# Kernel optimization log

Measured on AMD Instinct MI355X. Metric: run time of the kernel, lower is better.

Reference implementation:

```python
import jax, jax.numpy as jnp
import numpy as np

D_MODEL = 1024
N_HEADS = 16
HEAD_DIM = D_MODEL // N_HEADS


def setup_inputs() -> dict:
    key = jax.random.key(0)
    ks = jax.random.split(key, 9)
    B, S, D = 2, 2048, D_MODEL
    scale = 1.0 / np.sqrt(D)
    return {
        "q": jax.random.normal(ks[0], (B, S, D), jnp.float32),
        "k": jax.random.normal(ks[1], (B, S, D), jnp.float32),
        "v": jax.random.normal(ks[2], (B, S, D), jnp.float32),
        "Wq": jax.random.normal(ks[3], (D, D), jnp.float32) * scale,
        "bq": jax.random.normal(ks[4], (D,), jnp.float32) * 0.01,
        "Wk": jax.random.normal(ks[5], (D, D), jnp.float32) * scale,
        "bk": jax.random.normal(ks[6], (D,), jnp.float32) * 0.01,
        "Wv": jax.random.normal(ks[7], (D, D), jnp.float32) * scale,
        "bv": jax.random.normal(ks[8], (D,), jnp.float32) * 0.01,
    }


def reference(q, k, v, Wq, bq, Wk, bk, Wv, bv):
    B, S, D = q.shape
    H, Dh = N_HEADS, D // N_HEADS
    # linear projections (torch Linear: x @ W.T + b)
    qp = q @ Wq.T + bq
    kp = k @ Wk.T + bk
    vp = v @ Wv.T + bv
    # [B, S, H, Dh] -> [B, H, S, Dh]
    qh = qp.reshape(B, S, H, Dh).transpose(0, 2, 1, 3)
    kh = kp.reshape(B, S, H, Dh).transpose(0, 2, 1, 3)
    vh = vp.reshape(B, S, H, Dh).transpose(0, 2, 1, 3)
    # scaled dot-product attention (mask=None path)
    scores = jnp.einsum('bhqd,bhkd->bhqk', qh, kh) / jnp.sqrt(jnp.asarray(Dh, qh.dtype))
    attn = jax.nn.softmax(scores, axis=-1)
    out = jnp.einsum('bhqk,bhkd->bhqd', attn, vh)
    # [B, H, S, Dh] -> [B, S, D]
    return out.transpose(0, 2, 1, 3).reshape(B, S, D)
```

## Files before the change

### kernel.cpp

```cpp
#include <hip/hip_runtime.h>
#include <stdint.h>
#include <stddef.h>


#define NH  16
#define DH  64
#define SEQ 2048
#define DM  1024
#define NB  2

#define ACT_N (NB * SEQ * DM)
#define W_N   (DM * DM)
#define QSCALE 0.18033688011116012f

typedef float  f32x4  __attribute__((ext_vector_type(4)));
typedef __bf16 bf16x8 __attribute__((ext_vector_type(8)));
typedef __bf16 bf16x4 __attribute__((ext_vector_type(4)));

__device__ __forceinline__ __bf16 f2bf(float f) { return (__bf16)f; }

__device__ __forceinline__ float fexp2(float x) {
    float r; asm("v_exp_f32 %0, %1" : "=v"(r) : "v"(x)); return r;
}

__device__ __forceinline__ void gload_lds16(const void* g, void* l) {
    __builtin_amdgcn_global_load_lds(
        (const __attribute__((address_space(1))) void*)g,
        (__attribute__((address_space(3))) void*)l, 16, 0, 0);
}

__global__ __launch_bounds__(256) void cvt6(
    const float* __restrict__ s0, const float* __restrict__ s1,
    const float* __restrict__ s2, const float* __restrict__ s3,
    const float* __restrict__ s4, const float* __restrict__ s5,
    __bf16* __restrict__ d0, __bf16* __restrict__ d1, __bf16* __restrict__ d2,
    __bf16* __restrict__ d3, __bf16* __restrict__ d4, __bf16* __restrict__ d5)
{
    const float* s; __bf16* d; int n;
    switch (blockIdx.z) {
        case 0: s = s0; d = d0; n = ACT_N; break;
        case 1: s = s1; d = d1; n = ACT_N; break;
        case 2: s = s2; d = d2; n = ACT_N; break;
        case 3: s = s3; d = d3; n = W_N;   break;
        case 4: s = s4; d = d4; n = W_N;   break;
        default: s = s5; d = d5; n = W_N;  break;
    }
    const size_t i = ((size_t)blockIdx.x * 256 + threadIdx.x) * 8;
    if (i >= (size_t)n) return;
    float4 f0 = *(const float4*)(s + i);
    float4 f1 = *(const float4*)(s + i + 4);
    bf16x8 o;
    o[0] = f2bf(f0.x); o[1] = f2bf(f0.y); o[2] = f2bf(f0.z); o[3] = f2bf(f0.w);
    o[4] = f2bf(f1.x); o[5] = f2bf(f1.y); o[6] = f2bf(f1.z); o[7] = f2bf(f1.w);
    *(bf16x8*)(d + i) = o;
}

__global__ __launch_bounds__(256) void proj3(
    const __bf16* __restrict__ X0, const __bf16* __restrict__ X1, const __bf16* __restrict__ X2,
    const __bf16* __restrict__ W0, const __bf16* __restrict__ W1, const __bf16* __restrict__ W2,
    const float* __restrict__ b0, const float* __restrict__ b1, const float* __restrict__ b2,
    __bf16* __restrict__ dq, __bf16* __restrict__ dk, __bf16* __restrict__ dv)
{
    __shared__ __align__(16) __bf16 sA[3][128][32];
    __shared__ __align__(16) __bf16 sB[3][128][32];

    const __bf16 *X, *W; const float* bias; __bf16* dst;
    if (blockIdx.z == 0)      { X = X0; W = W0; bias = b0; dst = dq; }
    else if (blockIdx.z == 1) { X = X1; W = W1; bias = b1; dst = dk; }
    else                      { X = X2; W = W2; bias = b2; dst = dv; }
    const bool vpath = (blockIdx.z == 2);

    const int lane = threadIdx.x & 63;
    const int wv   = threadIdx.x >> 6;
    const int mb = blockIdx.x * 128;
    const int nb = blockIdx.y * 128;
    const int lm0 = (wv >> 1) * 64;
    const int ln0 = (wv & 1) * 64;
    const int lr = lane & 15;
    const int lg = lane >> 4;
    const int lk = lg * 8;
    const int srow = lane >> 2;
    const int scol = (lane & 3) * 8;

    const __bf16* xs = X + (size_t)(mb + wv * 32 + srow) * DM + scol;
    const __bf16* ws = W + (size_t)(nb + wv * 32 + srow) * DM + scol;

#define PSTAGE(SL, T) { \
    gload_lds16(xs + (size_t)(T) * 32,                  &sA[SL][wv * 32][0]); \
    gload_lds16(xs + (size_t)(T) * 32 + (size_t)16 * DM, &sA[SL][wv * 32 + 16][0]); \
    gload_lds16(ws + (size_t)(T) * 32,                  &sB[SL][wv * 32][0]); \
    gload_lds16(ws + (size_t)(T) * 32 + (size_t)16 * DM, &sB[SL][wv * 32 + 16][0]); }

    f32x4 acc[4][4];
#pragma unroll
    for (int i = 0; i < 4; ++i)
#pragma unroll
        for (int j = 0; j < 4; ++j) acc[i][j] = (f32x4){0.f, 0.f, 0.f, 0.f};

    PSTAGE(0, 0);
    PSTAGE(1, 1);

#pragma unroll
    for (int t = 0; t < 32; ++t) {
        __syncthreads();
        if (t + 2 < 32) PSTAGE((t + 2) % 3, t + 2);

        const int sl = t % 3;
        bf16x8 a[4], b[4];
#pragma unroll
        for (int f = 0; f < 4; ++f) {
            a[f] = *(const bf16x8*)&sA[sl][lm0 + f * 16 + lr][lk];
            b[f] = *(const bf16x8*)&sB[sl][ln0 + f * 16 + lr][lk];
        }
        __builtin_amdgcn_s_setprio(1);
        if (!vpath) {
#pragma unroll
            for (int nt = 0; nt < 4; ++nt)
#pragma unroll
                for (int mt = 0; mt < 4; ++mt)
                    acc[nt][mt] = __builtin_amdgcn_mfma_f32_16x16x32_bf16(
                        b[nt], a[mt], acc[nt][mt], 0, 0, 0);
        } else {
#pragma unroll
            for (int mt = 0; mt < 4; ++mt)
#pragma unroll
                for (int nt = 0; nt < 4; ++nt)
                    acc[mt][nt] = __builtin_amdgcn_mfma_f32_16x16x32_bf16(
                        a[mt], b[nt], acc[mt][nt], 0, 0, 0);
        }
        __builtin_amdgcn_s_setprio(0);
    }
#undef PSTAGE

    if (!vpath) {
        const float scale = (blockIdx.z == 0) ? QSCALE : 1.0f;
#pragma unroll
        for (int nt = 0; nt < 4; ++nt) {
            const int n_base = nb + ln0 + nt * 16 + lg * 4;
            const float4 bb = *(const float4*)&bias[n_base];
            const int h = n_base >> 6, dh = n_base & 63;
#pragma unroll
            for (int mt = 0; mt < 4; ++mt) {
                const int m_g = mb + lm0 + mt * 16 + lr;
                const int bi = m_g >> 11;
                const int s  = m_g & (SEQ - 1);
                bf16x4 w;
                w[0] = f2bf((acc[nt][mt][0] + bb.x) * scale);
                w[1] = f2bf((acc[nt][mt][1] + bb.y) * scale);
                w[2] = f2bf((acc[nt][mt][2] + bb.z) * scale);
                w[3] = f2bf((acc[nt][mt][3] + bb.w) * scale);
                *(bf16x4*)&dst[((size_t)((bi * NH + h) * SEQ + s)) * DH + dh] = w;
            }
        }
    } else {
        const int h = (nb + ln0) >> 6;
#pragma unroll
        for (int nt = 0; nt < 4; ++nt) {
            const int n_g = nb + ln0 + nt * 16 + lr;
            const float bb = bias[n_g];
            const int dh = n_g & 63;
#pragma unroll
            for (int mt = 0; mt < 4; ++mt) {
                const int m_g = mb + lm0 + mt * 16 + lg * 4;
                const int bi = m_g >> 11;
                const int s0 = m_g & (SEQ - 1);
                bf16x4 w;
#pragma unroll
                for (int r = 0; r < 4; ++r) w[r] = f2bf(acc[mt][nt][r] + bb);
                *(bf16x4*)&dst[((size_t)((bi * NH + h) * DH + dh)) * SEQ + s0] = w;
            }
        }
    }
}

__global__ __launch_bounds__(256) void attn_kernel(
    const __bf16* __restrict__ qh, const __bf16* __restrict__ kh,
    const __bf16* __restrict__ vT, float* __restrict__ out)
{
    __shared__ __align__(16) __bf16 kbuf[3][4096];
    __shared__ __align__(16) __bf16 vbuf[3][4096];

    const int tid  = threadIdx.x;
    const int lane = tid & 63;
    const int wv   = tid >> 6;
    const int i    = blockIdx.x;
    const int slot = i >> 3;
    const int bh   = (i & 7) * 4 + (slot >> 4);
    const int qt   = slot & 15;
    const size_t hb = (size_t)bh * SEQ * DH;
    const int q0 = qt * 128 + wv * 32;
    const int lq = lane & 15;
    const int lg = lane >> 4;
    const int swz = (lq & 7) << 4;

    const int p0 = tid, p1 = tid + 256;
    const int c0 = (p0 ^ ((p0 >> 3) & 7)) & 7;
    const int c1 = (p1 ^ ((p1 >> 3) & 7)) & 7;
    const int r0 = p0 >> 3, r1 = p1 >> 3;
    const int gr0 = (r0 & 35) | ((r0 & 12) << 1) | ((r0 & 16) >> 2);
    const int gr1 = (r1 & 35) | ((r1 & 12) << 1) | ((r1 & 16) >> 2);
    const __bf16* ks0 = kh + hb + (size_t)gr0 * DH + c0 * 8;
    const __bf16* ks1 = kh + hb + (size_t)gr1 * DH + c1 * 8;
    const __bf16* vs0 = vT + hb + (size_t)r0 * SEQ + c0 * 8;
    const __bf16* vs1 = vT + hb + (size_t)r1 * SEQ + c1 * 8;
    const int dst0 = wv * 512;
    const int dst1 = 2048 + wv * 512;

#define STAGE(SEL, TI) { \
    gload_lds16(ks0 + (size_t)(TI) * 64 * DH, &kbuf[SEL][dst0]); \
    gload_lds16(ks1 + (size_t)(TI) * 64 * DH, &kbuf[SEL][dst1]); \
    gload_lds16(vs0 + (TI) * 64, &vbuf[SEL][dst0]); \
    gload_lds16(vs1 + (TI) * 64, &vbuf[SEL][dst1]); }

    bf16x8 bQ[2][2];
#pragma unroll
    for (int qtf = 0; qtf < 2; ++qtf)
#pragma unroll
        for (int ks = 0; ks < 2; ++ks)
            bQ[qtf][ks] = *(const bf16x8*)(qh + hb +
                (size_t)(q0 + qtf * 16 + lq) * DH + ks * 32 + lg * 8);

    bf16x8 ONES;
#pragma unroll
    for (int e = 0; e < 8; ++e) ONES[e] = f2bf(1.0f);

    f32x4 O[2][4];
#pragma unroll
    for (int qtf = 0; qtf < 2; ++qtf)
#pragma unroll
        for (int dt = 0; dt < 4; ++dt) O[qtf][dt] = (f32x4){0.f, 0.f, 0.f, 0.f};
    f32x4 Ol[2];
    Ol[0] = (f32x4){0.f, 0.f, 0.f, 0.f};
    Ol[1] = (f32x4){0.f, 0.f, 0.f, 0.f};

    const int rdk0 = lq * 128 + ((0 * 64 + lg * 16) ^ swz);
    const int rdk1 = lq * 128 + ((1 * 64 + lg * 16) ^ swz);

    f32x4 scA[2][4], scB[2][4];
    bf16x8 paf[2][2];

#define QK(SL, SC) { \
    const char* kc = (const char*)&kbuf[SL][0]; \
    _Pragma("unroll") for (int kt = 0; kt < 4; ++kt) { \
        const bf16x8 ak0 = *(const bf16x8*)(kc + kt * 2048 + rdk0); \
        const bf16x8 ak1 = *(const bf16x8*)(kc + kt * 2048 + rdk1); \
        _Pragma("unroll") for (int qtf = 0; qtf < 2; ++qtf) { \
            f32x4 c = (f32x4){0.f, 0.f, 0.f, 0.f}; \
            c = __builtin_amdgcn_mfma_f32_16x16x32_bf16(ak0, bQ[qtf][0], c, 0, 0, 0); \
            c = __builtin_amdgcn_mfma_f32_16x16x32_bf16(ak1, bQ[qtf][1], c, 0, 0, 0); \
            SC[qtf][kt] = c; } } }

#define SMAX(SC) { \
    _Pragma("unroll") for (int qtf = 0; qtf < 2; ++qtf) \
    _Pragma("unroll") for (int ks = 0; ks < 2; ++ks) { \
        bf16x8 w; \
        _Pragma("unroll") for (int r = 0; r < 4; ++r) { \
            w[r]     = f2bf(fexp2(SC[qtf][2 * ks][r])); \
            w[4 + r] = f2bf(fexp2(SC[qtf][2 * ks + 1][r])); } \
        paf[qtf][ks] = w; } }

#define PV(SL) { \
    const char* vc = (const char*)&vbuf[SL][0]; \
    _Pragma("unroll") for (int ks = 0; ks < 2; ++ks) { \
        const int rd = (ks == 0) ? rdk0 : rdk1; \
        _Pragma("unroll") for (int dt = 0; dt < 4; ++dt) { \
            const bf16x8 bv = *(const bf16x8*)(vc + dt * 2048 + rd); \
            O[0][dt] = __builtin_amdgcn_mfma_f32_16x16x32_bf16(paf[0][ks], bv, O[0][dt], 0, 0, 0); \
            O[1][dt] = __builtin_amdgcn_mfma_f32_16x16x32_bf16(paf[1][ks], bv, O[1][dt], 0, 0, 0); } \
        Ol[0] = __builtin_amdgcn_mfma_f32_16x16x32_bf16(paf[0][ks], ONES, Ol[0], 0, 0, 0); \
        Ol[1] = __builtin_amdgcn_mfma_f32_16x16x32_bf16(paf[1][ks], ONES, Ol[1], 0, 0, 0); } }

#define BODY(T, SCUR, SNXT) { \
    SMAX(SCUR); \
    __syncthreads(); \
    if ((T) + 2 < 32) STAGE(((T) + 2) % 3, (T) + 2); \
    __builtin_amdgcn_s_setprio(1); \
    if ((T) + 1 < 32) QK(((T) + 1) % 3, SNXT); \
    PV((T) % 3); \
    __builtin_amdgcn_s_setprio(0); }

    STAGE(0, 0);
    STAGE(1, 1);
    __syncthreads();
    QK(0, scA);

#pragma unroll
    for (int t = 0; t < 32; t += 2) {
        BODY(t, scA, scB);
        BODY(t + 1, scB, scA);
    }
#undef BODY
#undef PV
#undef SMAX
#undef QK
#undef STAGE

    const int b = bh >> 4, h = bh & 15;
#pragma unroll
    for (int qtf = 0; qtf < 2; ++qtf) {
#pragma unroll
        for (int r = 0; r < 4; ++r) {
            const float li = 1.0f / (qtf ? Ol[1][r] : Ol[0][r]);
            const int s_g = q0 + qtf * 16 + lg * 4 + r;
            float* op = out + ((size_t)(b * SEQ + s_g)) * DM + h * DH;
#pragma unroll
            for (int dt = 0; dt < 4; ++dt)
                op[dt * 16 + lq] = O[qtf][dt][r] * li;
        }
    }
}

extern "C" void kernel_launch(void* const* d_in, const int* in_sizes, int n_in,
                              void* d_out, int out_size, void* d_ws, size_t ws_size,
                              hipStream_t stream)
{
    (void)in_sizes; (void)n_in; (void)out_size; (void)ws_size;
    const float* q  = (const float*)d_in[0];
    const float* k  = (const float*)d_in[1];
    const float* v  = (const float*)d_in[2];
    const float* Wq = (const float*)d_in[3];
    const float* bq = (const float*)d_in[4];
    const float* Wk = (const float*)d_in[5];
    const float* bk = (const float*)d_in[6];
    const float* Wv = (const float*)d_in[7];
    const float* bv = (const float*)d_in[8];

    const size_t act = (size_t)ACT_N;
    const size_t wn  = (size_t)W_N;
    __bf16* qx  = (__bf16*)d_ws;
    __bf16* kx  = qx + act;
    __bf16* vx  = kx + act;
    __bf16* wqb = vx + act;
    __bf16* wkb = wqb + wn;
    __bf16* wvb = wkb + wn;
    __bf16* qhd = wvb + wn;
    __bf16* khd = qhd + act;
    __bf16* vhd = khd + act;
    float* out = (float*)d_out;

    cvt6<<<dim3(2048, 1, 6), dim3(256), 0, stream>>>(
        q, k, v, Wq, Wk, Wv, qx, kx, vx, wqb, wkb, wvb);
    proj3<<<dim3(32, 8, 3), dim3(256), 0, stream>>>(
        qx, kx, vx, wqb, wkb, wvb, bq, bk, bv, qhd, khd, vhd);
    attn_kernel<<<dim3(512), dim3(256), 0, stream>>>(qhd, khd, vhd, out);
}
```

Measured before the change: 102.0 us.

## Deepen attention K/V pipeline, swizzle projection LDS, use partial vmcnt waits

The projection GEMM's LDS tiles are flattened and XOR-swizzled on both the global-to-LDS store and the fragment reads, to cut bank conflicts. Both kernels replace __syncthreads with a partial s_waitcnt vmcnt followed by a raw s_barrier, so newer prefetches can stay in flight. The attention kernel goes from triple to quadruple buffering of K/V, prefetching three tiles ahead. This uses more LDS, which may lower occupancy, and correctness depends on the vmcnt counts matching the number of outstanding loads.

```diff
diff --git a/kernel.cpp b/kernel.cpp
--- a/kernel.cpp
+++ b/kernel.cpp
@@ -28,6 +28,8 @@
         (const __attribute__((address_space(1))) void*)g,
         (__attribute__((address_space(3))) void*)l, 16, 0, 0);
 }
+
+#define WAITVM(N) asm volatile("s_waitcnt vmcnt(" #N ")" ::: "memory")
 
 __global__ __launch_bounds__(256) void cvt6(
     const float* __restrict__ s0, const float* __restrict__ s1,
@@ -61,8 +63,8 @@
     const float* __restrict__ b0, const float* __restrict__ b1, const float* __restrict__ b2,
     __bf16* __restrict__ dq, __bf16* __restrict__ dk, __bf16* __restrict__ dv)
 {
-    __shared__ __align__(16) __bf16 sA[3][128][32];
-    __shared__ __align__(16) __bf16 sB[3][128][32];
+    __shared__ __align__(16) __bf16 sA[3][4096];
+    __shared__ __align__(16) __bf16 sB[3][4096];
 
     const __bf16 *X, *W; const float* bias; __bf16* dst;
     if (blockIdx.z == 0)      { X = X0; W = W0; bias = b0; dst = dq; }
@@ -78,18 +80,19 @@
     const int ln0 = (wv & 1) * 64;
     const int lr = lane & 15;
     const int lg = lane >> 4;
-    const int lk = lg * 8;
+
     const int srow = lane >> 2;
-    const int scol = (lane & 3) * 8;
-
+    const int scol = (((lane & 3) ^ ((lane >> 3) & 3))) * 8;
     const __bf16* xs = X + (size_t)(mb + wv * 32 + srow) * DM + scol;
     const __bf16* ws = W + (size_t)(nb + wv * 32 + srow) * DM + scol;
 
 #define PSTAGE(SL, T) { \
-    gload_lds16(xs + (size_t)(T) * 32,                  &sA[SL][wv * 32][0]); \
-    gload_lds16(xs + (size_t)(T) * 32 + (size_t)16 * DM, &sA[SL][wv * 32 + 16][0]); \
-    gload_lds16(ws + (size_t)(T) * 32,                  &sB[SL][wv * 32][0]); \
-    gload_lds16(ws + (size_t)(T) * 32 + (size_t)16 * DM, &sB[SL][wv * 32 + 16][0]); }
+    gload_lds16(xs + (size_t)(T) * 32,                   &sA[SL][wv * 1024]); \
+    gload_lds16(xs + (size_t)(T) * 32 + (size_t)16 * DM, &sA[SL][wv * 1024 + 512]); \
+    gload_lds16(ws + (size_t)(T) * 32,                   &sB[SL][wv * 1024]); \
+    gload_lds16(ws + (size_t)(T) * 32 + (size_t)16 * DM, &sB[SL][wv * 1024 + 512]); }
+
+    const int rchunk = (lg ^ ((lr >> 1) & 3)) * 8;
 
     f32x4 acc[4][4];
 #pragma unroll
@@ -102,15 +105,16 @@
 
 #pragma unroll
     for (int t = 0; t < 32; ++t) {
-        __syncthreads();
+        if (t <= 30) { WAITVM(4); } else { WAITVM(0); }
+        __builtin_amdgcn_s_barrier();
         if (t + 2 < 32) PSTAGE((t + 2) % 3, t + 2);
 
         const int sl = t % 3;
         bf16x8 a[4], b[4];
 #pragma unroll
         for (int f = 0; f < 4; ++f) {
-            a[f] = *(const bf16x8*)&sA[sl][lm0 + f * 16 + lr][lk];
-            b[f] = *(const bf16x8*)&sB[sl][ln0 + f * 16 + lr][lk];
+            a[f] = *(const bf16x8*)&sA[sl][(lm0 + f * 16 + lr) * 32 + rchunk];
+            b[f] = *(const bf16x8*)&sB[sl][(ln0 + f * 16 + lr) * 32 + rchunk];
         }
         __builtin_amdgcn_s_setprio(1);
         if (!vpath) {
@@ -177,8 +181,8 @@
     const __bf16* __restrict__ qh, const __bf16* __restrict__ kh,
     const __bf16* __restrict__ vT, float* __restrict__ out)
 {
-    __shared__ __align__(16) __bf16 kbuf[3][4096];
-    __shared__ __align__(16) __bf16 vbuf[3][4096];
+    __shared__ __align__(16) __bf16 kbuf[4][4096];
+    __shared__ __align__(16) __bf16 vbuf[4][4096];
 
     const int tid  = threadIdx.x;
     const int lane = tid & 63;
@@ -272,16 +276,19 @@
 
 #define BODY(T, SCUR, SNXT) { \
     SMAX(SCUR); \
-    __syncthreads(); \
-    if ((T) + 2 < 32) STAGE(((T) + 2) % 3, (T) + 2); \
+    if ((T) <= 29) { WAITVM(4); } else { WAITVM(0); } \
+    __builtin_amdgcn_s_barrier(); \
+    if ((T) + 3 < 32) STAGE(((T) + 3) & 3, (T) + 3); \
     __builtin_amdgcn_s_setprio(1); \
-    if ((T) + 1 < 32) QK(((T) + 1) % 3, SNXT); \
-    PV((T) % 3); \
+    if ((T) + 1 < 32) QK(((T) + 1) & 3, SNXT); \
+    PV((T) & 3); \
     __builtin_amdgcn_s_setprio(0); }
 
     STAGE(0, 0);
     STAGE(1, 1);
-    __syncthreads();
+    STAGE(2, 2);
+    WAITVM(8);
+    __builtin_amdgcn_s_barrier();
     QK(0, scA);
 
 #pragma unroll
```

Result: no change. 101.5 us (-0.5%).
